# Kernel optimization log

Measured on AMD Instinct MI355X. Metric: run time of the kernel, lower is better.

The kernel has to match this reference:

```python
import jax, jax.numpy as jnp
import numpy as np

B, S, D = 8, 512, 512
IN_S = IN_D = IN_E = 32
OUT_S = OUT_D = OUT_E = 32


def setup_inputs() -> dict:
    key = jax.random.key(0)
    ks = jax.random.split(key, 16)
    sc = 0.1
    return {
        "x_s": jax.random.normal(ks[0], (B, S, IN_S), jnp.float32),
        "x_d": jax.random.normal(ks[1], (B, D, IN_D), jnp.float32),
        "x_e": jax.random.normal(ks[2], (B, S, D, IN_E), jnp.float32),
        "W_ss": jax.random.normal(ks[3], (OUT_S, IN_S), jnp.float32) * sc,
        "b_ss": jnp.zeros((OUT_S,), jnp.float32),
        "W_se": jax.random.normal(ks[4], (OUT_S, IN_E), jnp.float32) * sc,
        "a_se_w": jax.random.normal(ks[5], (IN_E,), jnp.float32) * sc,
        "a_se_b": jnp.zeros((), jnp.float32),
        "W_dd": jax.random.normal(ks[6], (OUT_D, IN_D), jnp.float32) * sc,
        "b_dd": jnp.zeros((OUT_D,), jnp.float32),
        "W_de": jax.random.normal(ks[7], (OUT_D, IN_E), jnp.float32) * sc,
        "a_de_w": jax.random.normal(ks[8], (IN_E,), jnp.float32) * sc,
        "a_de_b": jnp.zeros((), jnp.float32),
        "W_ee": jax.random.normal(ks[9], (OUT_E, IN_E), jnp.float32) * sc,
        "b_ee": jnp.zeros((OUT_E,), jnp.float32),
        "W_es": jax.random.normal(ks[10], (OUT_E, IN_S), jnp.float32) * sc,
        "W_ed": jax.random.normal(ks[11], (OUT_E, IN_D), jnp.float32) * sc,
    }


def reference(x_s, x_d, x_e, W_ss, b_ss, W_se, a_se_w, a_se_b,
              W_dd, b_dd, W_de, a_de_w, a_de_b, W_ee, b_ee, W_es, W_ed):
    # Supply update: attention softmax over demand axis (dim=2)
    att_s = jax.nn.softmax(jnp.einsum('bsde,e->bsd', x_e, a_se_w) + a_se_b, axis=2)
    proj_se = jnp.einsum('bsde,oe->bsdo', x_e, W_se)
    h_s = jnp.einsum('bsi,oi->bso', x_s, W_ss) + b_ss \
        + jnp.einsum('bsdo,bsd->bso', proj_se, att_s)

    # Demand update: attention softmax over supply axis (dim=1)
    att_d = jax.nn.softmax(jnp.einsum('bsde,e->bsd', x_e, a_de_w) + a_de_b, axis=1)
    proj_de = jnp.einsum('bsde,oe->bsdo', x_e, W_de)
    h_d = jnp.einsum('bdi,oi->bdo', x_d, W_dd) + b_dd \
        + jnp.einsum('bsdo,bsd->bdo', proj_de, att_d)

    # Edge update: edge linear + broadcast node projections
    h_e = jnp.einsum('bsde,oe->bsdo', x_e, W_ee) + b_ee \
        + jnp.einsum('bsi,oi->bso', x_s, W_es)[:, :, None, :] \
        + jnp.einsum('bdi,oi->bdo', x_d, W_ed)[:, None, :, :]
    return (h_s, h_d, h_e)
```

## Files before the change

kernel.cpp:

```cpp
#include <hip/hip_runtime.h>
#include <cstddef>

#define B_ 8
#define S_ 512
#define D_ 512
#define TS 8
#define NST 64
#define DH 128
#define NZ 4

#define WS_BASES 0
#define WS_PES   131072
#define WS_BASED 262144
#define WS_PED   393216
#define WS_UD    524288
#define WS_ZD    (WS_UD + B_*NST*D_*32)
#define WS_US    (WS_ZD + B_*NST*D_)
#define WS_ZS    (WS_US + B_*S_*NZ*32)

#define HS_OFF 0
#define HD_OFF 131072
#define HE_OFF 262144

__global__ __launch_bounds__(256)
void k0_nodes(const float* __restrict__ x_s, const float* __restrict__ x_d,
              const float* __restrict__ W_ss, const float* __restrict__ b_ss,
              const float* __restrict__ W_dd, const float* __restrict__ b_dd,
              const float* __restrict__ W_es, const float* __restrict__ W_ed,
              float* __restrict__ ws)
{
  int g = blockIdx.x * 256 + threadIdx.x;
  int row = g >> 5, o = g & 31;
  bool sup = row < (B_ * S_);
  int r = sup ? row : row - B_ * S_;
  const float* x  = (sup ? x_s : x_d) + r * 32;
  const float* W1 = sup ? W_ss : W_dd;
  const float* W2 = sup ? W_es : W_ed;
  const float* bb = sup ? b_ss : b_dd;
  float xr[32];
#pragma unroll
  for (int k = 0; k < 8; k++)
    *(float4*)&xr[4*k] = *(const float4*)(x + 4*k);
  float acc1 = bb[o], acc2 = 0.f;
#pragma unroll
  for (int e = 0; e < 32; e++) {
    acc1 += xr[e] * W1[o*32 + e];
    acc2 += xr[e] * W2[o*32 + e];
  }
  int ob = sup ? WS_BASES : WS_BASED;
  int op = sup ? WS_PES  : WS_PED;
  ws[ob + r*32 + o] = acc1;
  ws[op + r*32 + o] = acc2;
}

__global__ __launch_bounds__(256, 4)
void k1_main(const float* __restrict__ x_e,
             const float* __restrict__ a_se_w, const float* __restrict__ a_se_b,
             const float* __restrict__ a_de_w, const float* __restrict__ a_de_b,
             const float* __restrict__ W_ee, const float* __restrict__ b_ee,
             float* __restrict__ ws,
             float* __restrict__ out)
{
  __shared__ float lds_ud[DH * 33];
  __shared__ float lds_hb[TS * 32];

  const int t = threadIdx.x;
  const int s_idx = t >> 5, d_off = t & 31;
  const int st = blockIdx.x, b = blockIdx.y, z = blockIdx.z;
  const int s = st * TS + s_idx;
  const int d0 = z * DH;

  for (int idx = t; idx < DH * 33; idx += 256) lds_ud[idx] = 0.f;
  lds_hb[t] = ws[WS_PES + (b*S_ + st*TS + (t>>5))*32 + (t&31)] + b_ee[t&31];
  __syncthreads();

  const float* xrow  = x_e + ((size_t)(b * S_ + s) * D_ + d0) * 32;
  float*       herow = out + HE_OFF + ((size_t)(b * S_ + s) * D_ + d0) * 32;
  const float* peD   = ws + WS_PED + ((size_t)b * D_ + d0) * 32;

  float us_acc[32];
#pragma unroll
  for (int e = 0; e < 32; e++) us_acc[e] = 0.f;
  float zs_acc = 0.f;
  const float asb = a_se_b[0], adb = a_de_b[0];

  float4 xb[8];
#pragma unroll
  for (int k = 0; k < 8; k++)
    xb[k] = *(const float4*)(xrow + d_off*32 + 4*k);

#pragma unroll 1
  for (int i = 0; i < 4; i++) {
    const int d = i*32 + d_off;
    float x[32];
#pragma unroll
    for (int k = 0; k < 8; k++) {
      x[4*k+0] = xb[k].x; x[4*k+1] = xb[k].y;
      x[4*k+2] = xb[k].z; x[4*k+3] = xb[k].w;
    }
    const int dn = (i < 3) ? d + 32 : d;
#pragma unroll
    for (int k = 0; k < 8; k++)
      xb[k] = *(const float4*)(xrow + dn*32 + 4*k);

    float ls = asb, ldt = adb;
#pragma unroll
    for (int e = 0; e < 32; e++) {
      ls  += x[e] * a_se_w[e];
      ldt += x[e] * a_de_w[e];
    }
    float es = __expf(ls), ed = __expf(ldt);
    zs_acc += es;
#pragma unroll
    for (int e = 0; e < 32; e++) us_acc[e] += es * x[e];

#pragma unroll
    for (int oq = 0; oq < 8; oq++) {
      float4 pdq = *(const float4*)(peD + d*32 + 4*oq);
      float4 hb  = *(const float4*)&lds_hb[s_idx*32 + 4*oq];
      float a0 = 0.f, a1 = 0.f, a2 = 0.f, a3 = 0.f;
#pragma unroll
      for (int e = 0; e < 32; e++) {
        a0 += x[e] * W_ee[(4*oq+0)*32 + e];
        a1 += x[e] * W_ee[(4*oq+1)*32 + e];
        a2 += x[e] * W_ee[(4*oq+2)*32 + e];
        a3 += x[e] * W_ee[(4*oq+3)*32 + e];
      }
      float4 r;
      r.x = a0 + hb.x + pdq.x;
      r.y = a1 + hb.y + pdq.y;
      r.z = a2 + hb.z + pdq.z;
      r.w = a3 + hb.w + pdq.w;
      *(float4*)(herow + d*32 + 4*oq) = r;
    }

#pragma unroll
    for (int e = 0; e < 32; e++)
      atomicAdd(&lds_ud[d*33 + e], ed * x[e]);
    atomicAdd(&lds_ud[d*33 + 32], ed);
  }
  __syncthreads();

  float* wud = ws + WS_UD + ((size_t)(b * NST + st) * D_ + d0) * 32;
  float* wzd = ws + WS_ZD + (b * NST + st) * D_ + d0;
#pragma unroll 1
  for (int sw = 0; sw < 4; sw++) {
    int r = sw * 32 + (t >> 3), g = t & 7;
    *(float4*)(wud + r*32 + g*4) = *(float4*)&lds_ud[r*33 + g*4];
  }
  if (t < DH) wzd[t] = lds_ud[t*33 + 32];
  __syncthreads();

  float* red = lds_ud;
  if (t < 128) {
#pragma unroll
    for (int k = 0; k < 8; k++) {
      float4 v;
      v.x = us_acc[4*k+0]; v.y = us_acc[4*k+1];
      v.z = us_acc[4*k+2]; v.w = us_acc[4*k+3];
      *(float4*)&red[t*33 + 4*k] = v;
    }
    red[t*33 + 32] = zs_acc;
  }
  __syncthreads();
  if (t < 128) {
    float sum = 0.f, zsum = 0.f;
#pragma unroll 1
    for (int dd = 0; dd < 32; dd++) {
      sum  += red[(s_idx*32 + dd)*33 + d_off];
      zsum += red[(s_idx*32 + dd)*33 + 32];
    }
    ws[WS_US + ((size_t)(b*S_ + s) * NZ + z) * 32 + d_off] = sum;
    if (d_off == 0) ws[WS_ZS + (b*S_ + s)*NZ + z] = zsum;
  }
  __syncthreads();
  if (t >= 128) {
    const int tl = t - 128;
#pragma unroll
    for (int k = 0; k < 8; k++) {
      float4 v;
      v.x = us_acc[4*k+0]; v.y = us_acc[4*k+1];
      v.z = us_acc[4*k+2]; v.w = us_acc[4*k+3];
      *(float4*)&red[tl*33 + 4*k] = v;
    }
    red[tl*33 + 32] = zs_acc;
  }
  __syncthreads();
  if (t >= 128) {
    const int sl = s_idx - 4;
    float sum = 0.f, zsum = 0.f;
#pragma unroll 1
    for (int dd = 0; dd < 32; dd++) {
      sum  += red[(sl*32 + dd)*33 + d_off];
      zsum += red[(sl*32 + dd)*33 + 32];
    }
    ws[WS_US + ((size_t)(b*S_ + s) * NZ + z) * 32 + d_off] = sum;
    if (d_off == 0) ws[WS_ZS + (b*S_ + s)*NZ + z] = zsum;
  }
}

__global__ __launch_bounds__(256)
void k2_tail(const float* __restrict__ W_de, const float* __restrict__ W_se,
             const float* __restrict__ ws, float* __restrict__ out)
{
  __shared__ float lds_u[8 * 32];
  const int t = threadIdx.x;
  const int r = t >> 5, e = t & 31;

  if (blockIdx.x < 512) {
    const int b = blockIdx.x >> 6, dg = blockIdx.x & 63;
    const int d = dg * 8 + r;
    const float* wud = ws + WS_UD;
    const float* wzd = ws + WS_ZD;
    float sum = 0.f, zv = 0.f;
#pragma unroll 4
    for (int st = 0; st < NST; st++) {
      sum += wud[((size_t)(b*NST + st) * D_ + d) * 32 + e];
      zv  += wzd[(b*NST + st) * D_ + d];
    }
    lds_u[r*32 + e] = sum / zv;
    __syncthreads();
    float acc = ws[WS_BASED + (b*D_ + d)*32 + e];
#pragma unroll
    for (int ee = 0; ee < 32; ee++)
      acc += W_de[e*32 + ee] * lds_u[r*32 + ee];
    out[HD_OFF + (b*D_ + d)*32 + e] = acc;
  } else {
    const int row = (blockIdx.x - 512) * 8 + r;
    float U = 0.f, Z = 0.f;
#pragma unroll
    for (int z = 0; z < NZ; z++) {
      U += ws[WS_US + ((size_t)row*NZ + z)*32 + e];
      Z += ws[WS_ZS + row*NZ + z];
    }
    lds_u[r*32 + e] = U / Z;
    __syncthreads();
    float acc = ws[WS_BASES + (size_t)row*32 + e];
#pragma unroll
    for (int ee = 0; ee < 32; ee++)
      acc += W_se[e*32 + ee] * lds_u[r*32 + ee];
    out[HS_OFF + (size_t)row*32 + e] = acc;
  }
}

extern "C" void kernel_launch(void* const* d_in, const int* in_sizes, int n_in,
                              void* d_out, int out_size, void* d_ws, size_t ws_size,
                              hipStream_t stream)
{
  const float* x_s    = (const float*)d_in[0];
  const float* x_d    = (const float*)d_in[1];
  const float* x_e    = (const float*)d_in[2];
  const float* W_ss   = (const float*)d_in[3];
  const float* b_ss   = (const float*)d_in[4];
  const float* W_se   = (const float*)d_in[5];
  const float* a_se_w = (const float*)d_in[6];
  const float* a_se_b = (const float*)d_in[7];
  const float* W_dd   = (const float*)d_in[8];
  const float* b_dd   = (const float*)d_in[9];
  const float* W_de   = (const float*)d_in[10];
  const float* a_de_w = (const float*)d_in[11];
  const float* a_de_b = (const float*)d_in[12];
  const float* W_ee   = (const float*)d_in[13];
  const float* b_ee   = (const float*)d_in[14];
  const float* W_es   = (const float*)d_in[15];
  const float* W_ed   = (const float*)d_in[16];
  float* out = (float*)d_out;
  float* ws  = (float*)d_ws;

  hipLaunchKernelGGL(k0_nodes, dim3(1024), dim3(256), 0, stream,
                     x_s, x_d, W_ss, b_ss, W_dd, b_dd, W_es, W_ed, ws);
  hipLaunchKernelGGL(k1_main, dim3(NST, B_, NZ), dim3(256), 0, stream,
                     x_e, a_se_w, a_se_b, a_de_w, a_de_b, W_ee, b_ee, ws, out);
  hipLaunchKernelGGL(k2_tail, dim3(1024), dim3(256), 0, stream, W_de, W_se, ws, out);
}
```

Before: 849.7 us.

## Reduce demand partials via global atomics instead of per-tile workspace

Each k1 block now atomically adds its per-demand partial sums and normalizers straight into one zeroed global buffer, instead of writing a separate slice per supply tile that k2 later reduces over 64 tiles. The buffer is zeroed in k0, and k2 only divides the accumulated values. This removes the large partial-sum writes and reads, at the cost of many global float atomics (64-way contention per address) and non-deterministic summation order. Launch bounds are also raised to 8 blocks per CU, which may force register spills given the large per-thread accumulator arrays.

```diff
diff --git a/kernel.cpp b/kernel.cpp
--- a/kernel.cpp
+++ b/kernel.cpp
@@ -14,9 +14,10 @@
 #define WS_BASED 262144
 #define WS_PED   393216
 #define WS_UD    524288
-#define WS_ZD    (WS_UD + B_*NST*D_*32)
-#define WS_US    (WS_ZD + B_*NST*D_)
+#define WS_ZD    (WS_UD + B_*D_*32)
+#define WS_US    (WS_ZD + B_*D_)
 #define WS_ZS    (WS_US + B_*S_*NZ*32)
+#define NZERO    (B_*D_*32 + B_*D_)
 
 #define HS_OFF 0
 #define HD_OFF 131072
@@ -30,6 +31,7 @@
               float* __restrict__ ws)
 {
   int g = blockIdx.x * 256 + threadIdx.x;
+  if (g < NZERO) ws[WS_UD + g] = 0.f;
   int row = g >> 5, o = g & 31;
   bool sup = row < (B_ * S_);
   int r = sup ? row : row - B_ * S_;
@@ -53,7 +55,7 @@
   ws[op + r*32 + o] = acc2;
 }
 
-__global__ __launch_bounds__(256, 4)
+__global__ __launch_bounds__(256, 8)
 void k1_main(const float* __restrict__ x_e,
              const float* __restrict__ a_se_w, const float* __restrict__ a_se_b,
              const float* __restrict__ a_de_w, const float* __restrict__ a_de_b,
@@ -141,14 +143,17 @@
   }
   __syncthreads();
 
-  float* wud = ws + WS_UD + ((size_t)(b * NST + st) * D_ + d0) * 32;
-  float* wzd = ws + WS_ZD + (b * NST + st) * D_ + d0;
-#pragma unroll 1
-  for (int sw = 0; sw < 4; sw++) {
-    int r = sw * 32 + (t >> 3), g = t & 7;
-    *(float4*)(wud + r*32 + g*4) = *(float4*)&lds_ud[r*33 + g*4];
-  }
-  if (t < DH) wzd[t] = lds_ud[t*33 + 32];
+  {
+    float* udg = ws + WS_UD + ((size_t)b * D_ + d0) * 32;
+    float* zdg = ws + WS_ZD + b * D_ + d0;
+    const int r = t >> 1, h = t & 1;
+    const float* src = &lds_ud[r*33 + h*16];
+    float* dst = udg + r*32 + h*16;
+#pragma unroll
+    for (int j = 0; j < 16; j++)
+      atomicAdd(&dst[j], src[j]);
+    if (h) atomicAdd(&zdg[r], lds_ud[r*33 + 32]);
+  }
   __syncthreads();
 
   float* red = lds_ud;
@@ -210,15 +215,8 @@
   if (blockIdx.x < 512) {
     const int b = blockIdx.x >> 6, dg = blockIdx.x & 63;
     const int d = dg * 8 + r;
-    const float* wud = ws + WS_UD;
-    const float* wzd = ws + WS_ZD;
-    float sum = 0.f, zv = 0.f;
-#pragma unroll 4
-    for (int st = 0; st < NST; st++) {
-      sum += wud[((size_t)(b*NST + st) * D_ + d) * 32 + e];
-      zv  += wzd[(b*NST + st) * D_ + d];
-    }
-    lds_u[r*32 + e] = sum / zv;
+    float u = ws[WS_UD + ((size_t)b*D_ + d)*32 + e] / ws[WS_ZD + b*D_ + d];
+    lds_u[r*32 + e] = u;
     __syncthreads();
     float acc = ws[WS_BASED + (b*D_ + d)*32 + e];
 #pragma unroll
```

Measured after the change: 1.450 ms. 70.7% more time.
